# Kernel tuning notes

Hardware: AMD Instinct MI355X
Metric: run time of the kernel (lower is better)

## Reference

```python
import jax, jax.numpy as jnp
import numpy as np

IMG_SIZE = 1536.0
NUM_ANCHORS = 145152  # 3*(48^2 + 96^2 + 192^2) for strides 32/16/8 at 1536px
NUM_CH = 85           # 4 box + 1 obj + 80 classes


def setup_inputs() -> dict:
    key = jax.random.key(0)
    k1, k2 = jax.random.split(key)
    predictions = jax.random.uniform(k1, (1, NUM_ANCHORS, NUM_CH), dtype=jnp.float32)
    score_threshold = jax.random.uniform(k2, (1,), dtype=jnp.float32)
    return {"predictions": predictions, "score_threshold": score_threshold}


def _yolo2xywh(bboxes):
    # center-x/y + w/h -> corner-ish (x1, y1, x2, y2) as in the torch helper
    x = bboxes[..., 0] - bboxes[..., 2] / 2
    y = bboxes[..., 1] - bboxes[..., 3] / 2
    w = bboxes[..., 0] + bboxes[..., 2] / 2
    h = bboxes[..., 1] + bboxes[..., 3] / 2
    return jnp.stack((x, y, w, h), axis=2)


def reference(predictions, score_threshold):
    # threshold=False path: static shapes, no data-dependent compaction
    cls = predictions[..., 5:]
    class_conf = jnp.max(cls, axis=2, keepdims=True)           # [1, N, 1]
    class_pred = jnp.argmax(cls, axis=2, keepdims=True)        # [1, N, 1] int
    bboxes = predictions[..., :4] / IMG_SIZE                   # [1, N, 4]
    objectness = predictions[..., 4]                           # [1, N]
    scores = objectness * class_conf[..., 0]                   # [1, N]
    bboxes = _yolo2xywh(bboxes)                                # [1, N, 4]
    detections = jnp.concatenate(
        (bboxes, class_conf, class_pred.astype(jnp.float32)), axis=2)  # [1, N, 6]
    return (bboxes[0], scores[0], class_pred[0, :, 0], detections)
```

## Files before the change

kernel.cpp:

```cpp
#include <hip/hip_runtime.h>


#define N_ANCH 145152
#define NCH 85
#define NCLS 80

constexpr float INV_IMG = 1.0f / 1536.0f;
constexpr int APB = 64;
constexpr int TPB = 64;
constexpr int NVEC = APB * NCH / 4;
constexpr int FULL_ITERS = NVEC / TPB;
constexpr int TAIL = NVEC - FULL_ITERS * TPB;

typedef const __attribute__((address_space(1))) void* gptr_t;
typedef __attribute__((address_space(3))) void* lptr_t;

__global__ __launch_bounds__(TPB)
void yolo_decode(const float* __restrict__ pred, float* __restrict__ out) {
    __shared__ float lds[APB * NCH];

    const int lane = threadIdx.x;
    const int blk  = blockIdx.x;

    const float4* __restrict__ gbase = (const float4*)(pred + (size_t)blk * (APB * NCH));
    float4* lbase = (float4*)lds;
    #pragma unroll
    for (int i = 0; i < FULL_ITERS; ++i) {
        __builtin_amdgcn_global_load_lds(
            (gptr_t)(gbase + i * TPB + lane),
            (lptr_t)(lbase + i * TPB + lane), 16, 0, 0);
    }
    if (lane < TAIL) {
        __builtin_amdgcn_global_load_lds(
            (gptr_t)(gbase + FULL_ITERS * TPB + lane),
            (lptr_t)(lbase + FULL_ITERS * TPB + lane), 16, 0, 0);
    }
    asm volatile("s_waitcnt vmcnt(0)" ::: "memory");
    __syncthreads();

    const float* __restrict__ p = lds + lane * NCH;
    const float bx = p[0], by = p[1], bw = p[2], bh = p[3], obj = p[4];

    float cmax = p[5];
    int cidx = 0;
    #pragma unroll
    for (int k = 1; k < NCLS; ++k) {
        const float v = p[5 + k];
        if (v > cmax) { cmax = v; cidx = k; }
    }

    const float cx = bx * INV_IMG;
    const float cy = by * INV_IMG;
    const float hw = bw * (INV_IMG * 0.5f);
    const float hh = bh * (INV_IMG * 0.5f);
    const float x0 = cx - hw, y0 = cy - hh;
    const float x1 = cx + hw, y1 = cy + hh;

    const int a = blk * APB + lane;
    const float score = obj * cmax;
    const float clsf = (float)cidx;

    ((float4*)out)[a] = make_float4(x0, y0, x1, y1);
    out[4 * N_ANCH + a] = score;
    out[5 * N_ANCH + a] = clsf;
    float2* det = (float2*)(out + 6 * (size_t)N_ANCH + (size_t)a * 6);
    det[0] = make_float2(x0, y0);
    det[1] = make_float2(x1, y1);
    det[2] = make_float2(cmax, clsf);
}

extern "C" void kernel_launch(void* const* d_in, const int* in_sizes, int n_in,
                              void* d_out, int out_size, void* d_ws, size_t ws_size,
                              hipStream_t stream) {
    const float* pred = (const float*)d_in[0];
    float* out = (float*)d_out;
    yolo_decode<<<N_ANCH / APB, TPB, 0, stream>>>(pred, out);
}
```

Baseline: 82.84 us.

## Replace LDS staging with direct per-thread vectorized row loads

Drops the global-to-LDS async staging and barrier. Each thread now loads its own 85-float row straight from global memory into registers with float4 loads, and the block size grows from 64 to 256 threads. This removes the LDS round trip and synchronisation. In exchange, each load instruction is strided across lanes rather than coalesced, and the float4 accesses are not 16-byte aligned because rows are 340 bytes long.

Result: slower. 89.89 us (+8.5%).

```diff
diff --git a/kernel.cpp b/kernel.cpp
--- a/kernel.cpp
+++ b/kernel.cpp
@@ -6,59 +6,41 @@
 #define NCLS 80
 
 constexpr float INV_IMG = 1.0f / 1536.0f;
-constexpr int APB = 64;
-constexpr int TPB = 64;
-constexpr int NVEC = APB * NCH / 4;
-constexpr int FULL_ITERS = NVEC / TPB;
-constexpr int TAIL = NVEC - FULL_ITERS * TPB;
-
-typedef const __attribute__((address_space(1))) void* gptr_t;
-typedef __attribute__((address_space(3))) void* lptr_t;
+constexpr int TPB = 256;
 
 __global__ __launch_bounds__(TPB)
 void yolo_decode(const float* __restrict__ pred, float* __restrict__ out) {
-    __shared__ float lds[APB * NCH];
+    const int a = blockIdx.x * TPB + threadIdx.x;
+    const float* __restrict__ p = pred + (size_t)a * NCH;
 
-    const int lane = threadIdx.x;
-    const int blk  = blockIdx.x;
+    float4 cls[20];
+    #pragma unroll
+    for (int j = 0; j < 20; ++j)
+        cls[j] = *(const float4*)(p + 5 + 4 * j);
+    const float4 bb = *(const float4*)(p);
+    const float obj = p[4];
 
-    const float4* __restrict__ gbase = (const float4*)(pred + (size_t)blk * (APB * NCH));
-    float4* lbase = (float4*)lds;
-    #pragma unroll
-    for (int i = 0; i < FULL_ITERS; ++i) {
-        __builtin_amdgcn_global_load_lds(
-            (gptr_t)(gbase + i * TPB + lane),
-            (lptr_t)(lbase + i * TPB + lane), 16, 0, 0);
-    }
-    if (lane < TAIL) {
-        __builtin_amdgcn_global_load_lds(
-            (gptr_t)(gbase + FULL_ITERS * TPB + lane),
-            (lptr_t)(lbase + FULL_ITERS * TPB + lane), 16, 0, 0);
-    }
-    asm volatile("s_waitcnt vmcnt(0)" ::: "memory");
-    __syncthreads();
-
-    const float* __restrict__ p = lds + lane * NCH;
-    const float bx = p[0], by = p[1], bw = p[2], bh = p[3], obj = p[4];
-
-    float cmax = p[5];
+    float cmax = cls[0].x;
     int cidx = 0;
     #pragma unroll
-    for (int k = 1; k < NCLS; ++k) {
-        const float v = p[5 + k];
-        if (v > cmax) { cmax = v; cidx = k; }
+    for (int j = 0; j < 20; ++j) {
+        const float v0 = cls[j].x, v1 = cls[j].y, v2 = cls[j].z, v3 = cls[j].w;
+        const int k = 4 * j;
+        if (v0 > cmax) { cmax = v0; cidx = k;     }
+        if (v1 > cmax) { cmax = v1; cidx = k + 1; }
+        if (v2 > cmax) { cmax = v2; cidx = k + 2; }
+        if (v3 > cmax) { cmax = v3; cidx = k + 3; }
     }
 
-    const float cx = bx * INV_IMG;
-    const float cy = by * INV_IMG;
-    const float hw = bw * (INV_IMG * 0.5f);
-    const float hh = bh * (INV_IMG * 0.5f);
+    const float cx = bb.x * INV_IMG;
+    const float cy = bb.y * INV_IMG;
+    const float hw = bb.z * (INV_IMG * 0.5f);
+    const float hh = bb.w * (INV_IMG * 0.5f);
     const float x0 = cx - hw, y0 = cy - hh;
     const float x1 = cx + hw, y1 = cy + hh;
 
-    const int a = blk * APB + lane;
     const float score = obj * cmax;
-    const float clsf = (float)cidx;
+    const float clsf  = (float)cidx;
 
     ((float4*)out)[a] = make_float4(x0, y0, x1, y1);
     out[4 * N_ANCH + a] = score;
@@ -74,5 +56,5 @@
                               hipStream_t stream) {
     const float* pred = (const float*)d_in[0];
     float* out = (float*)d_out;
-    yolo_decode<<<N_ANCH / APB, TPB, 0, stream>>>(pred, out);
+    yolo_decode<<<N_ANCH / TPB, TPB, 0, stream>>>(pred, out);
 }
```
